# Kernel optimization log

Hardware: AMD Instinct MI355X
Metric: run time of the kernel (lower is better)

The kernel has to match this reference:

```python
import jax, jax.numpy as jnp
import numpy as np

N = 8192
D_IN = 60
NUM_CLASSES = 10


def _xavier(key, out_f, in_f):
    limit = float(np.sqrt(6.0 / (in_f + out_f)))
    return jax.random.uniform(key, (out_f, in_f), jnp.float32, -limit, limit)


def setup_inputs() -> dict:
    key = jax.random.key(0)
    ks = jax.random.split(key, 10)
    return {
        "x": jax.random.normal(ks[0], (N, D_IN), jnp.float32),
        "fc1_w": _xavier(ks[1], 32, 60),
        "fc1_b": jnp.zeros((32,), jnp.float32),
        "fc2_w": _xavier(ks[2], 16, 32),
        "fc2_b": jnp.zeros((16,), jnp.float32),
        "fc3_w": _xavier(ks[3], 8, 60),
        "fc3_b": jnp.zeros((8,), jnp.float32),
        "fc6_w": _xavier(ks[4], NUM_CLASSES, 8),
        "fc6_b": jnp.zeros((NUM_CLASSES,), jnp.float32),
        "temp": jnp.float32(1.0) + 0.1 * jax.random.truncated_normal(ks[5], -2.0, 2.0, (), jnp.float32),
        "theta": jnp.float32(1.0) + 0.1 * jax.random.truncated_normal(ks[6], -2.0, 2.0, (), jnp.float32),
    }


def _pairwise_sq_dist(z):
    # z: [N, d] -> [N, N] squared euclidean distances, clamped at 0
    sq = jnp.sum(z * z, axis=1)  # [N]
    dist = sq[:, None] + sq[None, :] - 2.0 * (z @ z.T)
    return jnp.maximum(dist, 0.0)


def reference(x, fc1_w, fc1_b, fc2_w, fc2_b, fc3_w, fc3_b, fc6_w, fc6_b, temp, theta):
    net = x @ fc1_w.T + fc1_b           # [N, 32]
    net = net @ fc2_w.T + fc2_b         # [N, 16]
    A = -_pairwise_sq_dist(net)         # [N, N]
    A = jax.nn.sigmoid(temp * A + theta)
    # A * (1 - I) + I == set diagonal to 1
    A = jnp.fill_diagonal(A, 1.0, inplace=False)
    A = A / jnp.sum(A, axis=1, keepdims=True)
    h = A @ x                           # [N, 60] dense graph aggregation
    h = h @ fc3_w.T + fc3_b             # [N, 8]
    return jax.nn.softmax(h @ fc6_w.T + fc6_b, axis=1)  # [N, num_classes]
```

## Files before the change

kernel.cpp:

```cpp
#include <hip/hip_runtime.h>
#include <math.h>

#define NROWS 8192
#define DIN   60
#define DZ    16
#define NC    10

#define LOG2E 1.4426950408889634f

#define RB      128
#define CJ      512
#define NRB     (NROWS / RB)
#define NCH     (NROWS / CJ)
#define WAVES   4

typedef short    bf16x8 __attribute__((ext_vector_type(8)));
typedef float    f32x4  __attribute__((ext_vector_type(4)));
typedef float    f32x16 __attribute__((ext_vector_type(16)));
typedef unsigned u32x2  __attribute__((ext_vector_type(2)));

__device__ __forceinline__ unsigned int bfr(float f) {
    return (__float_as_uint(f) + 0x8000u) >> 16;
}

__global__ __launch_bounds__(64) void k1_all(
    const float* __restrict__ x,
    const float* __restrict__ w1, const float* __restrict__ b1,
    const float* __restrict__ w2, const float* __restrict__ b2,
    const float* __restrict__ temp_p, const float* __restrict__ theta_p,
    unsigned short* __restrict__ zb, float* __restrict__ bbf,
    unsigned short* __restrict__ xT)
{
    int i = blockIdx.x * 64 + threadIdx.x;

    float xr[DIN];
    const float4* xp = reinterpret_cast<const float4*>(x + (size_t)i * DIN);
    #pragma unroll
    for (int c = 0; c < 15; ++c) {
        float4 v = xp[c];
        xr[c*4+0] = v.x; xr[c*4+1] = v.y; xr[c*4+2] = v.z; xr[c*4+3] = v.w;
    }

    float n1[32];
    #pragma unroll
    for (int o = 0; o < 32; ++o) {
        float acc = b1[o];
        #pragma unroll
        for (int k = 0; k < DIN; ++k) acc = fmaf(w1[o*DIN+k], xr[k], acc);
        n1[o] = acc;
    }

    float z[DZ];
    float sq = 0.0f;
    #pragma unroll
    for (int u = 0; u < DZ; ++u) {
        float acc = b2[u];
        #pragma unroll
        for (int o = 0; o < 32; ++o) acc = fmaf(w2[u*32+o], n1[o], acc);
        z[u] = acc;
        sq = fmaf(acc, acc, sq);
    }

    float temp  = *temp_p;
    float theta = *theta_p;
    float s = sqrtf(2.0f * temp * LOG2E);

    unsigned int p[8];
    #pragma unroll
    for (int u = 0; u < 8; ++u) {
        unsigned int lo = bfr(z[2*u]   * s);
        unsigned int hi = bfr(z[2*u+1] * s);
        p[u] = lo | (hi << 16);
    }
    uint4* dst = reinterpret_cast<uint4*>(zb + (size_t)i * 16);
    dst[0] = make_uint4(p[0], p[1], p[2], p[3]);
    dst[1] = make_uint4(p[4], p[5], p[6], p[7]);

    bbf[i] = LOG2E * fmaf(temp, sq, -0.5f * theta);

    #pragma unroll
    for (int c = 0; c < DIN; ++c)
        xT[(size_t)c * NROWS + i] = (unsigned short)bfr(xr[c]);
    xT[(size_t)60 * NROWS + i] = 0x3F80;
    xT[(size_t)61 * NROWS + i] = 0;
    xT[(size_t)62 * NROWS + i] = 0;
    xT[(size_t)63 * NROWS + i] = 0;
}

__global__ __launch_bounds__(256) void k2_mfma(
    const unsigned short* __restrict__ zb, const float* __restrict__ bbf,
    const unsigned short* __restrict__ xT, const float* __restrict__ theta_p,
    float* __restrict__ hfin)
{
    const int tid  = threadIdx.x;
    const int lane = tid & 63, wave = tid >> 6;
    const int ic = lane & 31;
    const int h  = lane >> 5;
    const int rb = blockIdx.x & (NRB - 1);
    const int ch = blockIdx.x >> 6;
    const int it = rb * RB + wave * 32;
    const int j0 = ch * CJ;

    bf16x8 zbi = *reinterpret_cast<const bf16x8*>(zb + (size_t)(it + ic) * 16 + h * 8);
    const float bi = bbf[it + ic];
    const float nclamp = -(*theta_p) * LOG2E;

    const int  dd   = ic - 4 * h;
    const bool dl   = (dd >= 0) && ((dd & 7) < 4);
    const int  dreg = dl ? (((dd >> 3) << 2) | (dd & 3)) : -1;

    f32x16 z16;
    #pragma unroll
    for (int k = 0; k < 16; ++k) z16[k] = 0.0f;
    f32x16 H0 = z16, H1 = z16;

    for (int jb = 0; jb < CJ / 32; ++jb) {
        const int jt = j0 + jb * 32;
        bf16x8 za = *reinterpret_cast<const bf16x8*>(zb + (size_t)(jt + ic) * 16 + h * 8);
        f32x16 S = __builtin_amdgcn_mfma_f32_32x32x16_bf16(za, zbi, z16, 0, 0, 0);

        const bool dblk = (it == jt);
        unsigned pk[8];
        #pragma unroll
        for (int u = 0; u < 4; ++u) {
            f32x4 bj = *reinterpret_cast<const f32x4*>(bbf + jt + u * 8 + 4 * h);
            unsigned ur[4];
            #pragma unroll
            for (int r = 0; r < 4; ++r) {
                const int reg = u * 4 + r;
                float n = (bi + bj[r]) - S[reg];
                n = fmaxf(n, nclamp);
                float P = __builtin_amdgcn_rcpf(1.0f + __builtin_amdgcn_exp2f(n));
                if (dblk && reg == dreg) P = 0.0f;
                ur[r] = __float_as_uint(P) + 0x8000u;
            }
            pk[u*2 + 0] = (ur[0] >> 16) | (ur[1] & 0xFFFF0000u);
            pk[u*2 + 1] = (ur[2] >> 16) | (ur[3] & 0xFFFF0000u);
        }

        u32x2 sA = __builtin_amdgcn_permlane32_swap(pk[0], pk[2], false, false);
        u32x2 sB = __builtin_amdgcn_permlane32_swap(pk[1], pk[3], false, false);
        u32x2 sC = __builtin_amdgcn_permlane32_swap(pk[4], pk[6], false, false);
        u32x2 sD = __builtin_amdgcn_permlane32_swap(pk[5], pk[7], false, false);
        union { unsigned u[4]; bf16x8 v; } pa0, pa1;
        pa0.u[0] = sA[0]; pa0.u[1] = sB[0]; pa0.u[2] = sA[1]; pa0.u[3] = sB[1];
        pa1.u[0] = sC[0]; pa1.u[1] = sD[0]; pa1.u[2] = sC[1]; pa1.u[3] = sD[1];

        {
            bf16x8 xb0 = *reinterpret_cast<const bf16x8*>(
                xT + (size_t)(ic) * NROWS + jt + h*8);
            bf16x8 xb1 = *reinterpret_cast<const bf16x8*>(
                xT + (size_t)(ic) * NROWS + jt + 16 + h*8);
            H0 = __builtin_amdgcn_mfma_f32_32x32x16_bf16(pa0.v, xb0, H0, 0, 0, 0);
            H0 = __builtin_amdgcn_mfma_f32_32x32x16_bf16(pa1.v, xb1, H0, 0, 0, 0);
        }
        {
            bf16x8 xb0 = *reinterpret_cast<const bf16x8*>(
                xT + (size_t)(32 + ic) * NROWS + jt + h*8);
            bf16x8 xb1 = *reinterpret_cast<const bf16x8*>(
                xT + (size_t)(32 + ic) * NROWS + jt + 16 + h*8);
            H1 = __builtin_amdgcn_mfma_f32_32x32x16_bf16(pa0.v, xb0, H1, 0, 0, 0);
            H1 = __builtin_amdgcn_mfma_f32_32x32x16_bf16(pa1.v, xb1, H1, 0, 0, 0);
        }
    }

    #pragma unroll
    for (int reg = 0; reg < 16; ++reg) {
        const int row = it + (reg & 3) + 8 * (reg >> 2) + 4 * h;
        unsafeAtomicAdd(hfin + (size_t)row * 64 + ic,      H0[reg]);
        unsafeAtomicAdd(hfin + (size_t)row * 64 + 32 + ic, H1[reg]);
    }
}

__global__ __launch_bounds__(64) void k3_head(
    const float* __restrict__ x,
    const float* __restrict__ w3, const float* __restrict__ b3,
    const float* __restrict__ w6, const float* __restrict__ b6,
    const float* __restrict__ hfin,
    float* __restrict__ out)
{
    int i = blockIdx.x * 64 + threadIdx.x;

    const float* hi = hfin + (size_t)i * 64;
    const float* xi = x + (size_t)i * DIN;

    float rd = __builtin_amdgcn_rcpf(hi[60] + 1.0f);

    float h[DIN];
    #pragma unroll
    for (int k = 0; k < DIN; ++k) h[k] = (hi[k] + xi[k]) * rd;

    float g[8];
    #pragma unroll
    for (int o = 0; o < 8; ++o) {
        float a = b3[o];
        #pragma unroll
        for (int k = 0; k < DIN; ++k) a = fmaf(w3[o*DIN+k], h[k], a);
        g[o] = a;
    }

    float l[NC];
    float m = -3.0e38f;
    #pragma unroll
    for (int c = 0; c < NC; ++c) {
        float a = b6[c];
        #pragma unroll
        for (int o = 0; o < 8; ++o) a = fmaf(w6[c*8+o], g[o], a);
        l[c] = a;
        m = fmaxf(m, a);
    }
    float e[NC];
    float sum = 0.0f;
    #pragma unroll
    for (int c = 0; c < NC; ++c) {
        e[c] = __builtin_amdgcn_exp2f((l[c] - m) * LOG2E);
        sum += e[c];
    }
    float rsum = __builtin_amdgcn_rcpf(sum);
    #pragma unroll
    for (int c = 0; c < NC; ++c) out[(size_t)i * NC + c] = e[c] * rsum;
}

extern "C" void kernel_launch(void* const* d_in, const int* in_sizes, int n_in,
                              void* d_out, int out_size, void* d_ws, size_t ws_size,
                              hipStream_t stream)
{
    const float* x     = (const float*)d_in[0];
    const float* w1    = (const float*)d_in[1];
    const float* b1    = (const float*)d_in[2];
    const float* w2    = (const float*)d_in[3];
    const float* b2    = (const float*)d_in[4];
    const float* w3    = (const float*)d_in[5];
    const float* b3    = (const float*)d_in[6];
    const float* w6    = (const float*)d_in[7];
    const float* b6    = (const float*)d_in[8];
    const float* temp  = (const float*)d_in[9];
    const float* theta = (const float*)d_in[10];
    float* out = (float*)d_out;

    char* p = (char*)d_ws;
    unsigned short* zbuf = (unsigned short*)p;  p += (size_t)NROWS * 16 * 2;
    float*          bbf  = (float*)p;           p += (size_t)NROWS * 4;
    unsigned short* xT   = (unsigned short*)p;  p += (size_t)64 * NROWS * 2;
    float*          hfin = (float*)p;

    hipMemsetAsync(hfin, 0, (size_t)NROWS * 64 * sizeof(float), stream);
    k1_all <<<NROWS / 64, 64, 0, stream>>>(x, w1, b1, w2, b2, temp, theta, zbuf, bbf, xT);
    k2_mfma<<<NRB * NCH, 256, 0, stream>>>(zbuf, bbf, xT, theta, hfin);
    k3_head<<<NROWS / 64, 64, 0, stream>>>(x, w3, b3, w6, b6, hfin, out);
}
```

Baseline: 183.7 us.

## Fuse embed, pairwise, and head stages into one cooperative kernel with grid syncs

Combines the memset, embedding, pairwise MFMA aggregation and head kernels into a single cooperative launch of 1024 blocks, separated by grid-wide barriers. The aim is to remove the separate launch overheads and the inter-kernel gaps. In exchange, the embed and head phases now run on only 8 threads per 256-thread block, which leaves most lanes idle during those phases. The two grid syncs add their own cost, and the launch needs all 1024 blocks co-resident, with a fallback to the old four-launch path if the cooperative launch fails.

```diff
diff --git a/kernel.cpp b/kernel.cpp
--- a/kernel.cpp
+++ b/kernel.cpp
@@ -1,5 +1,8 @@
 #include <hip/hip_runtime.h>
+#include <hip/hip_cooperative_groups.h>
 #include <math.h>
+
+namespace cg = cooperative_groups;
 
 #define NROWS 8192
 #define DIN   60
@@ -12,7 +15,6 @@
 #define CJ      512
 #define NRB     (NROWS / RB)
 #define NCH     (NROWS / CJ)
-#define WAVES   4
 
 typedef short    bf16x8 __attribute__((ext_vector_type(8)));
 typedef float    f32x4  __attribute__((ext_vector_type(4)));
@@ -23,16 +25,14 @@
     return (__float_as_uint(f) + 0x8000u) >> 16;
 }
 
-__global__ __launch_bounds__(64) void k1_all(
-    const float* __restrict__ x,
+__device__ __forceinline__ void embed_row(
+    int i, const float* __restrict__ x,
     const float* __restrict__ w1, const float* __restrict__ b1,
     const float* __restrict__ w2, const float* __restrict__ b2,
-    const float* __restrict__ temp_p, const float* __restrict__ theta_p,
+    float temp, float theta,
     unsigned short* __restrict__ zb, float* __restrict__ bbf,
     unsigned short* __restrict__ xT)
 {
-    int i = blockIdx.x * 64 + threadIdx.x;
-
     float xr[DIN];
     const float4* xp = reinterpret_cast<const float4*>(x + (size_t)i * DIN);
     #pragma unroll
@@ -61,10 +61,7 @@
         sq = fmaf(acc, acc, sq);
     }
 
-    float temp  = *temp_p;
-    float theta = *theta_p;
     float s = sqrtf(2.0f * temp * LOG2E);
-
     unsigned int p[8];
     #pragma unroll
     for (int u = 0; u < 8; ++u) {
@@ -87,23 +84,23 @@
     xT[(size_t)63 * NROWS + i] = 0;
 }
 
-__global__ __launch_bounds__(256) void k2_mfma(
+__device__ __forceinline__ void pair_body(
+    int tid, int bid,
     const unsigned short* __restrict__ zb, const float* __restrict__ bbf,
-    const unsigned short* __restrict__ xT, const float* __restrict__ theta_p,
+    const unsigned short* __restrict__ xT, float theta,
     float* __restrict__ hfin)
 {
-    const int tid  = threadIdx.x;
     const int lane = tid & 63, wave = tid >> 6;
     const int ic = lane & 31;
     const int h  = lane >> 5;
-    const int rb = blockIdx.x & (NRB - 1);
-    const int ch = blockIdx.x >> 6;
+    const int rb = bid & (NRB - 1);
+    const int ch = bid >> 6;
     const int it = rb * RB + wave * 32;
     const int j0 = ch * CJ;
 
     bf16x8 zbi = *reinterpret_cast<const bf16x8*>(zb + (size_t)(it + ic) * 16 + h * 8);
     const float bi = bbf[it + ic];
-    const float nclamp = -(*theta_p) * LOG2E;
+    const float nclamp = -theta * LOG2E;
 
     const int  dd   = ic - 4 * h;
     const bool dl   = (dd >= 0) && ((dd & 7) < 4);
@@ -172,53 +169,114 @@
     }
 }
 
+__device__ __forceinline__ void head_row(
+    int i, const float* __restrict__ x,
+    const float* __restrict__ w3, const float* __restrict__ b3,
+    const float* __restrict__ w6, const float* __restrict__ b6,
+    const float* __restrict__ hfin, float* __restrict__ out)
+{
+    const float* hi = hfin + (size_t)i * 64;
+    const float* xi = x + (size_t)i * DIN;
+
+    float rd = __builtin_amdgcn_rcpf(hi[60] + 1.0f);
+
+    float h[DIN];
+    #pragma unroll
+    for (int k = 0; k < DIN; ++k) h[k] = (hi[k] + xi[k]) * rd;
+
+    float g[8];
+    #pragma unroll
+    for (int o = 0; o < 8; ++o) {
+        float a = b3[o];
+        #pragma unroll
+        for (int k = 0; k < DIN; ++k) a = fmaf(w3[o*DIN+k], h[k], a);
+        g[o] = a;
+    }
+
+    float l[NC];
+    float m = -3.0e38f;
+    #pragma unroll
+    for (int c = 0; c < NC; ++c) {
+        float a = b6[c];
+        #pragma unroll
+        for (int o = 0; o < 8; ++o) a = fmaf(w6[c*8+o], g[o], a);
+        l[c] = a;
+        m = fmaxf(m, a);
+    }
+    float e[NC];
+    float sum = 0.0f;
+    #pragma unroll
+    for (int c = 0; c < NC; ++c) {
+        e[c] = __builtin_amdgcn_exp2f((l[c] - m) * LOG2E);
+        sum += e[c];
+    }
+    float rsum = __builtin_amdgcn_rcpf(sum);
+    #pragma unroll
+    for (int c = 0; c < NC; ++c) out[(size_t)i * NC + c] = e[c] * rsum;
+}
+
+__global__ __launch_bounds__(256, 4) void mega(
+    const float* __restrict__ x,
+    const float* __restrict__ w1, const float* __restrict__ b1,
+    const float* __restrict__ w2, const float* __restrict__ b2,
+    const float* __restrict__ w3, const float* __restrict__ b3,
+    const float* __restrict__ w6, const float* __restrict__ b6,
+    const float* __restrict__ temp_p, const float* __restrict__ theta_p,
+    unsigned short* __restrict__ zb, float* __restrict__ bbf,
+    unsigned short* __restrict__ xT, float* __restrict__ hfin,
+    float* __restrict__ out)
+{
+    const int tid = threadIdx.x, bid = blockIdx.x;
+    cg::grid_group grid = cg::this_grid();
+
+    const float temp  = *temp_p;
+    const float theta = *theta_p;
+
+    if (tid < 128) {
+        reinterpret_cast<float4*>(hfin)[bid * 128 + tid] =
+            make_float4(0.0f, 0.0f, 0.0f, 0.0f);
+    }
+    if (tid < 8)
+        embed_row(bid * 8 + tid, x, w1, b1, w2, b2, temp, theta, zb, bbf, xT);
+
+    grid.sync();
+
+    pair_body(tid, bid, zb, bbf, xT, theta, hfin);
+
+    grid.sync();
+
+    if (tid < 8)
+        head_row(bid * 8 + tid, x, w3, b3, w6, b6, hfin, out);
+}
+
+__global__ __launch_bounds__(64) void k1_all(
+    const float* __restrict__ x,
+    const float* __restrict__ w1, const float* __restrict__ b1,
+    const float* __restrict__ w2, const float* __restrict__ b2,
+    const float* __restrict__ temp_p, const float* __restrict__ theta_p,
+    unsigned short* __restrict__ zb, float* __restrict__ bbf,
+    unsigned short* __restrict__ xT)
+{
+    int i = blockIdx.x * 64 + threadIdx.x;
+    embed_row(i, x, w1, b1, w2, b2, *temp_p, *theta_p, zb, bbf, xT);
+}
+
+__global__ __launch_bounds__(256) void k2_mfma(
+    const unsigned short* __restrict__ zb, const float* __restrict__ bbf,
+    const unsigned short* __restrict__ xT, const float* __restrict__ theta_p,
+    float* __restrict__ hfin)
+{
+    pair_body(threadIdx.x, blockIdx.x, zb, bbf, xT, *theta_p, hfin);
+}
+
 __global__ __launch_bounds__(64) void k3_head(
     const float* __restrict__ x,
     const float* __restrict__ w3, const float* __restrict__ b3,
     const float* __restrict__ w6, const float* __restrict__ b6,
-    const float* __restrict__ hfin,
-    float* __restrict__ out)
+    const float* __restrict__ hfin, float* __restrict__ out)
 {
     int i = blockIdx.x * 64 + threadIdx.x;
-
-    const float* hi = hfin + (size_t)i * 64;
-    const float* xi = x + (size_t)i * DIN;
-
-    float rd = __builtin_amdgcn_rcpf(hi[60] + 1.0f);
-
-    float h[DIN];
-    #pragma unroll
-    for (int k = 0; k < DIN; ++k) h[k] = (hi[k] + xi[k]) * rd;
-
-    float g[8];
-    #pragma unroll
-    for (int o = 0; o < 8; ++o) {
-        float a = b3[o];
-        #pragma unroll
-        for (int k = 0; k < DIN; ++k) a = fmaf(w3[o*DIN+k], h[k], a);
-        g[o] = a;
-    }
-
-    float l[NC];
-    float m = -3.0e38f;
-    #pragma unroll
-    for (int c = 0; c < NC; ++c) {
-        float a = b6[c];
-        #pragma unroll
-        for (int o = 0; o < 8; ++o) a = fmaf(w6[c*8+o], g[o], a);
-        l[c] = a;
-        m = fmaxf(m, a);
-    }
-    float e[NC];
-    float sum = 0.0f;
-    #pragma unroll
-    for (int c = 0; c < NC; ++c) {
-        e[c] = __builtin_amdgcn_exp2f((l[c] - m) * LOG2E);
-        sum += e[c];
-    }
-    float rsum = __builtin_amdgcn_rcpf(sum);
-    #pragma unroll
-    for (int c = 0; c < NC; ++c) out[(size_t)i * NC + c] = e[c] * rsum;
+    head_row(i, x, w3, b3, w6, b6, hfin, out);
 }
 
 extern "C" void kernel_launch(void* const* d_in, const int* in_sizes, int n_in,
@@ -244,8 +302,25 @@
     unsigned short* xT   = (unsigned short*)p;  p += (size_t)64 * NROWS * 2;
     float*          hfin = (float*)p;
 
-    hipMemsetAsync(hfin, 0, (size_t)NROWS * 64 * sizeof(float), stream);
-    k1_all <<<NROWS / 64, 64, 0, stream>>>(x, w1, b1, w2, b2, temp, theta, zbuf, bbf, xT);
-    k2_mfma<<<NRB * NCH, 256, 0, stream>>>(zbuf, bbf, xT, theta, hfin);
-    k3_head<<<NROWS / 64, 64, 0, stream>>>(x, w3, b3, w6, b6, hfin, out);
-}
+    const float *xp = x, *w1p = w1, *b1p = b1, *w2p = w2, *b2p = b2;
+    const float *w3p = w3, *b3p = b3, *w6p = w6, *b6p = b6;
+    const float *tpp = temp, *thp = theta;
+    unsigned short *zbp = zbuf, *xTp = xT;
+    float *bbp = bbf, *hfp = hfin, *op = out;
+    void* args[] = {
+        (void*)&xp, (void*)&w1p, (void*)&b1p, (void*)&w2p, (void*)&b2p,
+        (void*)&w3p, (void*)&b3p, (void*)&w6p, (void*)&b6p,
+        (void*)&tpp, (void*)&thp,
+        (void*)&zbp, (void*)&bbp, (void*)&xTp, (void*)&hfp, (void*)&op
+    };
+    hipError_t e = hipLaunchCooperativeKernel(
+        (void*)mega, dim3(1024), dim3(256), args, 0, stream);
+
+    if (e != hipSuccess) {
+        hipMemsetAsync(hfin, 0, (size_t)NROWS * 64 * sizeof(float), stream);
+        k1_all <<<NROWS / 64, 64, 0, stream>>>(x, w1, b1, w2, b2, temp, theta,
+                                               zbuf, bbf, xT);
+        k2_mfma<<<NRB * NCH, 256, 0, stream>>>(zbuf, bbf, xT, theta, hfin);
+        k3_head<<<NROWS / 64, 64, 0, stream>>>(x, w3, b3, w6, b6, hfin, out);
+    }
+}
```

After: 433.8 us. 136% more time.
